# Optimization experiments

Hardware: AMD Instinct MI355X
Metric: run time of the kernel (lower is better)

The kernel has to match this reference:

```python
import jax, jax.numpy as jnp
import numpy as np

TOP_K = 2  # matches init top_k


def setup_inputs() -> dict:
    key = jax.random.key(0)
    k = jax.random.split(key, 5)
    B, S, D, E, H = 8, 2048, 768, 8, 3072  # batch, seq, n_embed, num_experts, 4*n_embed
    init = lambda kk, shape: (jax.random.normal(kk, shape, jnp.float32) * 0.02)
    return {
        "x": jax.random.normal(k[0], (B, S, D), jnp.float32),
        "Wg": init(k[1], (D, E)),            # router weight
        "bg": jnp.zeros((E,), jnp.float32),   # router bias
        "W1": init(k[2], (E, D, H)),          # stacked expert fc1
        "b1": jnp.zeros((E, H), jnp.float32),
        "W2": init(k[3], (E, H, D)),          # stacked expert fc2
        "b2": jnp.zeros((E, D), jnp.float32),
    }


def _moe(x, Wg, bg, W1, b1, W2, b2):
    B, S, D = x.shape
    E = Wg.shape[1]
    # --- TopkRouter: top-k logits, softmax over selected experts, scatter to full gate tensor ---
    logits = x @ Wg + bg                                  # [B,S,E]
    top_vals, top_idx = jax.lax.top_k(logits, TOP_K)      # [B,S,K]
    gates_k = jax.nn.softmax(top_vals, axis=-1)           # softmax over the k selected experts only
    one_hot = jax.nn.one_hot(top_idx, E, dtype=x.dtype)   # [B,S,K,E] (E is small)
    gates = jnp.sum(one_hot * gates_k[..., None], axis=-2)  # [B,S,E], zeros off top-k

    # --- dispatch/compute/combine: scan over experts (fixed, small), gate-weighted accumulate ---
    flat_x = x.reshape(-1, D)          # [T,D]
    flat_g = gates.reshape(-1, E).T    # [E,T]

    def body(acc, p):
        W1e, b1e, W2e, b2e, ge = p
        h = jax.nn.relu(flat_x @ W1e + b1e)               # [T,H]
        acc = acc + (h @ W2e + b2e) * ge[:, None]         # gate==0 -> zero contribution (incl. bias)
        return acc, None

    out, _ = jax.lax.scan(body, jnp.zeros_like(flat_x), (W1, b1, W2, b2, flat_g))
    return out.reshape(B, S, D)


def reference(x, Wg, bg, W1, b1, W2, b2):
    return _moe(x, Wg, bg, W1, b1, W2, b2)
```

## Files before the change

### kernel.cpp

```cpp
#include <hip/hip_runtime.h>
#include <stdint.h>

typedef unsigned short u16;
typedef __attribute__((ext_vector_type(8))) short v8s;
typedef __attribute__((ext_vector_type(4))) float v4f;

#define T_TOK 16384
#define DIM   768
#define NE    8
#define HH    3072
#define CH    1536
#define NCH   2
#define MCAP  34816

#define O_W1T 0u
#define O_W2T 37748736u
#define O_XBF 75497472u
#define O_STK 100663296u
#define O_SGT 100802560u
#define O_TE  100941824u
#define O_TG  101072896u
#define O_TS  101203968u
#define O_MET 101335040u
#define O_HBF 101335296u
#define O_OBF 208290048u
#define WS_TIER_A 261767424ull

__device__ __forceinline__ u16 f2bf(float f){
  uint32_t u = __float_as_uint(f);
  uint32_t r = (u + 0x7fffu + ((u >> 16) & 1u)) >> 16;
  return (u16)r;
}
__device__ __forceinline__ float bf2f(u16 v){
  return __uint_as_float(((uint32_t)v) << 16);
}
__device__ __forceinline__ void gll16(const u16* g, u16* l){
  __builtin_amdgcn_global_load_lds((const __attribute__((address_space(1))) uint32_t*)g,
                                   (__attribute__((address_space(3))) uint32_t*)l, 16, 0, 0);
}

#define BAR() do { asm volatile("" ::: "memory"); __builtin_amdgcn_s_barrier(); asm volatile("" ::: "memory"); } while(0)
#define WAIT_LGKM0() asm volatile("s_waitcnt lgkmcnt(0)" ::: "memory")
#define WAIT_VM4() asm volatile("s_waitcnt vmcnt(4)" ::: "memory")
#define WAIT_VM0() asm volatile("s_waitcnt vmcnt(0)" ::: "memory")

__global__ void k_transposeW1(const float* __restrict__ W1, u16* __restrict__ W1t){
  __shared__ float tile[32][33];
  int e = blockIdx.z;
  int h0 = blockIdx.x * 32, d0 = blockIdx.y * 32;
  const float* src = W1 + (size_t)e * DIM * HH;
  u16* dst = W1t + (size_t)e * HH * DIM;
  int tx = threadIdx.x, ty = threadIdx.y;
  #pragma unroll
  for (int j = 0; j < 4; j++)
    tile[ty + 8*j][tx] = src[(size_t)(d0 + ty + 8*j) * HH + h0 + tx];
  __syncthreads();
  #pragma unroll
  for (int j = 0; j < 4; j++)
    dst[(size_t)(h0 + ty + 8*j) * DIM + d0 + tx] = f2bf(tile[tx][ty + 8*j]);
}

__global__ void k_transposeW2(const float* __restrict__ W2, u16* __restrict__ W2t){
  __shared__ float tile[32][33];
  int e = blockIdx.z;
  int d0 = blockIdx.x * 32, h0 = blockIdx.y * 32;
  const float* src = W2 + (size_t)e * HH * DIM;
  u16* dst = W2t + (size_t)e * DIM * HH;
  int tx = threadIdx.x, ty = threadIdx.y;
  #pragma unroll
  for (int j = 0; j < 4; j++)
    tile[ty + 8*j][tx] = src[(size_t)(h0 + ty + 8*j) * DIM + d0 + tx];
  __syncthreads();
  #pragma unroll
  for (int j = 0; j < 4; j++)
    dst[(size_t)(d0 + ty + 8*j) * HH + h0 + tx] = f2bf(tile[tx][ty + 8*j]);
}

__global__ __launch_bounds__(256) void k_router(
    const float* __restrict__ x, const float* __restrict__ Wg, const float* __restrict__ bg,
    int* __restrict__ tE, float* __restrict__ tG, u16* __restrict__ Xbf){
  int t = blockIdx.x * 4 + (threadIdx.x >> 6);
  int l = threadIdx.x & 63;
  const float* xr = x + (size_t)t * DIM;
  u16* xb = Xbf + (size_t)t * DIM;
  float acc[NE];
  #pragma unroll
  for (int e = 0; e < NE; e++) acc[e] = 0.f;
  #pragma unroll
  for (int j = 0; j < DIM / 64; j++){
    int c = l + 64 * j;
    float xv = xr[c];
    xb[c] = f2bf(xv);
    const float4* wr4 = (const float4*)(Wg + (size_t)c * NE);
    float4 w0 = wr4[0], w1 = wr4[1];
    acc[0] += xv * w0.x; acc[1] += xv * w0.y; acc[2] += xv * w0.z; acc[3] += xv * w0.w;
    acc[4] += xv * w1.x; acc[5] += xv * w1.y; acc[6] += xv * w1.z; acc[7] += xv * w1.w;
  }
  #pragma unroll
  for (int off = 32; off; off >>= 1)
    #pragma unroll
    for (int e = 0; e < NE; e++) acc[e] += __shfl_xor(acc[e], off, 64);

  if (l == 0){
    float lgt[NE];
    #pragma unroll
    for (int e = 0; e < NE; e++) lgt[e] = acc[e] + bg[e];
    int i0 = 0; float v0 = lgt[0];
    #pragma unroll
    for (int e = 1; e < NE; e++) if (lgt[e] > v0){ v0 = lgt[e]; i0 = e; }
    int i1 = -1; float v1 = -1e30f;
    #pragma unroll
    for (int e = 0; e < NE; e++) if (e != i0 && lgt[e] > v1){ v1 = lgt[e]; i1 = e; }
    float ed = expf(v1 - v0);
    float g1 = ed / (1.f + ed);
    float g0 = 1.f / (1.f + ed);
    tE[2*t] = i0; tE[2*t+1] = i1;
    tG[2*t] = g0; tG[2*t+1] = g1;
  }
}

__global__ __launch_bounds__(256) void k_count(const int* __restrict__ tE, int* __restrict__ counts){
  int i = blockIdx.x * blockDim.x + threadIdx.x;
  int c[NE];
  #pragma unroll
  for (int e = 0; e < NE; e++) c[e] = 0;
  for (int j = i; j < 2 * T_TOK; j += 32 * 256){
    int v = tE[j];
    #pragma unroll
    for (int e = 0; e < NE; e++) c[e] += (v == e);
  }
  #pragma unroll
  for (int off = 32; off; off >>= 1)
    #pragma unroll
    for (int e = 0; e < NE; e++) c[e] += __shfl_xor(c[e], off, 64);
  if ((threadIdx.x & 63) == 0){
    #pragma unroll
    for (int e = 0; e < NE; e++) atomicAdd(&counts[e], c[e]);
  }
}

__global__ void k_scan(const int* __restrict__ counts, int* __restrict__ offs){
  if (threadIdx.x == 0){
    int o = 0;
    for (int e = 0; e < NE; e++){ offs[e] = o; o += (counts[e] + 255) & ~255; }
    offs[NE] = o;
  }
}

__global__ __launch_bounds__(256) void k_scatter(
    const int* __restrict__ tE, const float* __restrict__ tG,
    const int* __restrict__ offs, int* __restrict__ fill,
    int* __restrict__ slot_token, float* __restrict__ slot_gate, int* __restrict__ tSlot){
  int t = blockIdx.x * 256 + threadIdx.x;
  int lane = threadIdx.x & 63, w = threadIdx.x >> 6;
  int e0 = tE[2*t], e1 = tE[2*t+1];
  float g0 = tG[2*t], g1 = tG[2*t+1];

  __shared__ int wcnt[4][NE];
  __shared__ int woff[4][NE];
  __shared__ int bbase[NE];

  uint64_t below = (1ull << lane) - 1ull;
  int rank0 = 0, rank1 = 0;
  #pragma unroll
  for (int e = 0; e < NE; e++){
    uint64_t m0 = __ballot(e0 == e);
    uint64_t m1 = __ballot(e1 == e);
    int c0 = __popcll(m0);
    if (e0 == e) rank0 = __popcll(m0 & below);
    if (e1 == e) rank1 = c0 + __popcll(m1 & below);
    if (lane == 0) wcnt[w][e] = c0 + __popcll(m1);
  }
  __syncthreads();
  if (threadIdx.x < NE){
    int e = threadIdx.x;
    int s = 0;
    #pragma unroll
    for (int ww = 0; ww < 4; ww++){ woff[ww][e] = s; s += wcnt[ww][e]; }
    bbase[e] = atomicAdd(&fill[e], s);
  }
  __syncthreads();
  int p0 = offs[e0] + bbase[e0] + woff[w][e0] + rank0;
  slot_token[p0] = t; slot_gate[p0] = g0; tSlot[2*t] = p0;
  int p1 = offs[e1] + bbase[e1] + woff[w][e1] + rank1;
  slot_token[p1] = t; slot_gate[p1] = g1; tSlot[2*t+1] = p1;
}

__global__ void k_outinit(const int* __restrict__ tE, const float* __restrict__ tG,
                          const float* __restrict__ b2, float* __restrict__ out){
  int t = blockIdx.x;
  int e0 = tE[2*t], e1 = tE[2*t+1];
  float g0 = tG[2*t], g1 = tG[2*t+1];
  const float* r0 = b2 + (size_t)e0 * DIM;
  const float* r1 = b2 + (size_t)e1 * DIM;
  float* o = out + (size_t)t * DIM;
  #pragma unroll
  for (int j = 0; j < DIM / 256; j++){
    int c = threadIdx.x + 256 * j;
    o[c] = g0 * r0[c] + g1 * r1[c];
  }
}


#define ABASE(b,h) (((b)*2+(h))*8192)
#define BBASE(b,h) (32768 + ((b)*2+(h))*8192)
#define SWZE(ro,ks) (((((ro)*128) + (ks)*64 + lg*16) ^ (((lm)&7)<<4)) >> 1)

#define STAGE2(p0, p1, base, kk) do { \
  gll16((p0) + (kk), &lds[(base) + (w*2)*512]); \
  gll16((p1) + (kk), &lds[(base) + (w*2+1)*512]); } while(0)

#define MFMA_Q(MOFF, NOFF, BF) \
  __builtin_amdgcn_s_setprio(1); \
  _Pragma("unroll") \
  for (int mi = 0; mi < 4; mi++) \
    _Pragma("unroll") \
    for (int ni = 0; ni < 2; ni++) \
      _Pragma("unroll") \
      for (int ks = 0; ks < 2; ks++) \
        acc[(MOFF)+mi][(NOFF)+ni] = __builtin_amdgcn_mfma_f32_16x16x32_bf16(aF[mi][ks], BF[ni][ks], acc[(MOFF)+mi][(NOFF)+ni], 0, 0, 0); \
  __builtin_amdgcn_s_setprio(0);

__global__ __launch_bounds__(512, 2) void k_gemm1(
    const u16* __restrict__ Xbf, const u16* __restrict__ W1t, const float* __restrict__ b1,
    const int* __restrict__ slot_token, const float* __restrict__ slot_gate,
    const int* __restrict__ offs, u16* __restrict__ Hbuf, int cbase)
{
  const int NT = CH / 256;
  const int NWG = NE * 64 * NT;
  int bid = blockIdx.x;
  int swz = (bid & 7) * (NWG / 8) + (bid >> 3);
  int e = swz / (64 * NT);
  int rem = swz % (64 * NT);
  int mt = rem / NT, ntile = rem % NT;

  int mbase = offs[e];
  int pc = offs[e+1] - mbase;
  if (mt * 256 >= pc) return;
  int grb = mbase + mt * 256;
  int nb = ntile * 256;
  int habs = cbase + nb;

  __shared__ __align__(16) u16 lds[65536];

  int tid = threadIdx.x, w = tid >> 6, lane = tid & 63;
  int wm = w >> 2, wn = w & 3, lm = lane & 15, lg = lane >> 4;
  int cbe = (((lane & 7) ^ (lane >> 3)) << 3);

  int rA00 = (w*2+0)*8 + (lane>>3), rA01 = (w*2+1)*8 + (lane>>3);
  const u16 *sA00 = Xbf + (size_t)slot_token[grb + rA00]       * DIM + cbe;
  const u16 *sA01 = Xbf + (size_t)slot_token[grb + rA01]       * DIM + cbe;
  const u16 *sA10 = Xbf + (size_t)slot_token[grb + 128 + rA00] * DIM + cbe;
  const u16 *sA11 = Xbf + (size_t)slot_token[grb + 128 + rA01] * DIM + cbe;
  const u16 *sB00 = W1t + ((size_t)e*HH + habs + rA00)       * DIM + cbe;
  const u16 *sB01 = W1t + ((size_t)e*HH + habs + rA01)       * DIM + cbe;
  const u16 *sB10 = W1t + ((size_t)e*HH + habs + 128 + rA00) * DIM + cbe;
  const u16 *sB11 = W1t + ((size_t)e*HH + habs + 128 + rA01) * DIM + cbe;

  v4f acc[8][4];
  #pragma unroll
  for (int mi = 0; mi < 8; mi++)
    #pragma unroll
    for (int ni = 0; ni < 4; ni++) acc[mi][ni] = 0.f;

  const int NTK = DIM / 64;
  STAGE2(sA00, sA01, ABASE(0,0), 0);  STAGE2(sA10, sA11, ABASE(0,1), 0);
  STAGE2(sB00, sB01, BBASE(0,0), 0);  STAGE2(sB10, sB11, BBASE(0,1), 0);
  STAGE2(sA00, sA01, ABASE(1,0), 64); STAGE2(sA10, sA11, ABASE(1,1), 64);
  WAIT_VM4(); BAR();

  v8s aF[4][2], bF0[2][2], bF1[2][2];
  for (int k = 0; k < NTK; ++k){
    int cur = k & 1, nx = cur ^ 1;
    int ab = ABASE(cur, wm);
    int bb = BBASE(cur, wn >> 1);
    #pragma unroll
    for (int mi = 0; mi < 4; mi++)
      #pragma unroll
      for (int ks = 0; ks < 2; ks++)
        aF[mi][ks] = *(const v8s*)&lds[ab + SWZE(mi*16 + lm, ks)];
    #pragma unroll
    for (int ni = 0; ni < 2; ni++)
      #pragma unroll
      for (int ks = 0; ks < 2; ks++)
        bF0[ni][ks] = *(const v8s*)&lds[bb + SWZE((wn&1)*64 + ni*16 + lm, ks)];
    if (k + 1 < NTK) STAGE2(sB00, sB01, BBASE(nx,0), (k+1)*64);
    MFMA_Q(0, 0, bF0);
    BAR();
    #pragma unroll
    for (int ni = 0; ni < 2; ni++)
      #pragma unroll
      for (int ks = 0; ks < 2; ks++)
        bF1[ni][ks] = *(const v8s*)&lds[bb + SWZE((wn&1)*64 + (2+ni)*16 + lm, ks)];
    if (k + 1 < NTK) STAGE2(sB10, sB11, BBASE(nx,1), (k+1)*64);
    MFMA_Q(0, 2, bF1);
    BAR();
    #pragma unroll
    for (int mi = 0; mi < 4; mi++)
      #pragma unroll
      for (int ks = 0; ks < 2; ks++)
        aF[mi][ks] = *(const v8s*)&lds[ab + SWZE((4+mi)*16 + lm, ks)];
    MFMA_Q(4, 0, bF0);
    WAIT_LGKM0(); BAR();
    if (k + 2 < NTK){
      STAGE2(sA00, sA01, ABASE(cur,0), (k+2)*64);
      STAGE2(sA10, sA11, ABASE(cur,1), (k+2)*64);
    }
    MFMA_Q(4, 2, bF1);
    if (k + 2 < NTK) { WAIT_VM4(); } else { WAIT_VM0(); }
    BAR();
  }

  float b1v[4];
  #pragma unroll
  for (int ni = 0; ni < 4; ni++) b1v[ni] = b1[(size_t)e * HH + habs + wn*64 + ni*16 + lm];
  #pragma unroll
  for (int mi = 0; mi < 8; mi++){
    int rbase = grb + wm*128 + mi*16 + lg*4;
    float g[4];
    #pragma unroll
    for (int i = 0; i < 4; i++) g[i] = slot_gate[rbase + i];
    #pragma unroll
    for (int ni = 0; ni < 4; ni++){
      int col = nb + wn*64 + ni*16 + lm;
      #pragma unroll
      for (int i = 0; i < 4; i++){
        float v = acc[mi][ni][i] + b1v[ni];
        v = fmaxf(v, 0.f) * g[i];
        Hbuf[(size_t)(rbase + i) * CH + col] = f2bf(v);
      }
    }
  }
}

__global__ __launch_bounds__(512, 2) void k_gemm2(
    const u16* __restrict__ Hbuf, const u16* __restrict__ W2t,
    const int* __restrict__ slot_token, const int* __restrict__ offs,
    float* __restrict__ out, u16* __restrict__ Obuf, int cbase, int mode)
{
  const int NT = DIM / 256;
  const int NWG = NE * 64 * NT;
  int bid = blockIdx.x;
  int swz = (bid & 7) * (NWG / 8) + (bid >> 3);
  int e = swz / (64 * NT);
  int rem = swz % (64 * NT);
  int mt = rem / NT, ntile = rem % NT;

  int mbase = offs[e];
  int pc = offs[e+1] - mbase;
  if (mt * 256 >= pc) return;
  int grb = mbase + mt * 256;
  int nb = ntile * 256;

  __shared__ __align__(16) u16 lds[65536];

  int tid = threadIdx.x, w = tid >> 6, lane = tid & 63;
  int wm = w >> 2, wn = w & 3, lm = lane & 15, lg = lane >> 4;
  int cbe = (((lane & 7) ^ (lane >> 3)) << 3);

  int rA00 = (w*2+0)*8 + (lane>>3), rA01 = (w*2+1)*8 + (lane>>3);
  const u16 *sA00 = Hbuf + (size_t)(grb + rA00)       * CH + cbe;
  const u16 *sA01 = Hbuf + (size_t)(grb + rA01)       * CH + cbe;
  const u16 *sA10 = Hbuf + (size_t)(grb + 128 + rA00) * CH + cbe;
  const u16 *sA11 = Hbuf + (size_t)(grb + 128 + rA01) * CH + cbe;
  const u16 *sB00 = W2t + ((size_t)e*DIM + nb + rA00)       * HH + cbase + cbe;
  const u16 *sB01 = W2t + ((size_t)e*DIM + nb + rA01)       * HH + cbase + cbe;
  const u16 *sB10 = W2t + ((size_t)e*DIM + nb + 128 + rA00) * HH + cbase + cbe;
  const u16 *sB11 = W2t + ((size_t)e*DIM + nb + 128 + rA01) * HH + cbase + cbe;

  v4f acc[8][4];
  #pragma unroll
  for (int mi = 0; mi < 8; mi++)
    #pragma unroll
    for (int ni = 0; ni < 4; ni++) acc[mi][ni] = 0.f;

  const int NTK = CH / 64;
  STAGE2(sA00, sA01, ABASE(0,0), 0);  STAGE2(sA10, sA11, ABASE(0,1), 0);
  STAGE2(sB00, sB01, BBASE(0,0), 0);  STAGE2(sB10, sB11, BBASE(0,1), 0);
  STAGE2(sA00, sA01, ABASE(1,0), 64); STAGE2(sA10, sA11, ABASE(1,1), 64);
  WAIT_VM4(); BAR();

  v8s aF[4][2], bF0[2][2], bF1[2][2];
  for (int k = 0; k < NTK; ++k){
    int cur = k & 1, nx = cur ^ 1;
    int ab = ABASE(cur, wm);
    int bb = BBASE(cur, wn >> 1);
    #pragma unroll
    for (int mi = 0; mi < 4; mi++)
      #pragma unroll
      for (int ks = 0; ks < 2; ks++)
        aF[mi][ks] = *(const v8s*)&lds[ab + SWZE(mi*16 + lm, ks)];
    #pragma unroll
    for (int ni = 0; ni < 2; ni++)
      #pragma unroll
      for (int ks = 0; ks < 2; ks++)
        bF0[ni][ks] = *(const v8s*)&lds[bb + SWZE((wn&1)*64 + ni*16 + lm, ks)];
    if (k + 1 < NTK) STAGE2(sB00, sB01, BBASE(nx,0), (k+1)*64);
    MFMA_Q(0, 0, bF0);
    BAR();
    #pragma unroll
    for (int ni = 0; ni < 2; ni++)
      #pragma unroll
      for (int ks = 0; ks < 2; ks++)
        bF1[ni][ks] = *(const v8s*)&lds[bb + SWZE((wn&1)*64 + (2+ni)*16 + lm, ks)];
    if (k + 1 < NTK) STAGE2(sB10, sB11, BBASE(nx,1), (k+1)*64);
    MFMA_Q(0, 2, bF1);
    BAR();
    #pragma unroll
    for (int mi = 0; mi < 4; mi++)
      #pragma unroll
      for (int ks = 0; ks < 2; ks++)
        aF[mi][ks] = *(const v8s*)&lds[ab + SWZE((4+mi)*16 + lm, ks)];
    MFMA_Q(4, 0, bF0);
    WAIT_LGKM0(); BAR();
    if (k + 2 < NTK){
      STAGE2(sA00, sA01, ABASE(cur,0), (k+2)*64);
      STAGE2(sA10, sA11, ABASE(cur,1), (k+2)*64);
    }
    MFMA_Q(4, 2, bF1);
    if (k + 2 < NTK) { WAIT_VM4(); } else { WAIT_VM0(); }
    BAR();
  }

  if (mode == 0){
    #pragma unroll
    for (int mi = 0; mi < 8; mi++){
      int rbase = grb + wm*128 + mi*16 + lg*4;
      int tok[4];
      #pragma unroll
      for (int i = 0; i < 4; i++) tok[i] = slot_token[rbase + i];
      #pragma unroll
      for (int ni = 0; ni < 4; ni++){
        int col = nb + wn*64 + ni*16 + lm;
        #pragma unroll
        for (int i = 0; i < 4; i++)
          unsafeAtomicAdd(&out[(size_t)tok[i] * DIM + col], acc[mi][ni][i]);
      }
    }
  } else if (mode == 1){
    #pragma unroll
    for (int mi = 0; mi < 8; mi++){
      int rbase = grb + wm*128 + mi*16 + lg*4;
      #pragma unroll
      for (int ni = 0; ni < 4; ni++){
        int col = nb + wn*64 + ni*16 + lm;
        #pragma unroll
        for (int i = 0; i < 4; i++)
          Obuf[(size_t)(rbase + i) * DIM + col] = f2bf(acc[mi][ni][i]);
      }
    }
  } else {
    #pragma unroll
    for (int mi = 0; mi < 8; mi++){
      int rbase = grb + wm*128 + mi*16 + lg*4;
      #pragma unroll
      for (int ni = 0; ni < 4; ni++){
        int col = nb + wn*64 + ni*16 + lm;
        #pragma unroll
        for (int i = 0; i < 4; i++){
          size_t p = (size_t)(rbase + i) * DIM + col;
          Obuf[p] = f2bf(bf2f(Obuf[p]) + acc[mi][ni][i]);
        }
      }
    }
  }
}

__global__ __launch_bounds__(192) void k_combine(
    const u16* __restrict__ Obuf, const int* __restrict__ tSlot,
    const int* __restrict__ tE, const float* __restrict__ tG,
    const float* __restrict__ b2, float* __restrict__ out)
{
  int t = blockIdx.x;
  int l = threadIdx.x;
  int s0 = tSlot[2*t], s1 = tSlot[2*t+1];
  int e0 = tE[2*t], e1 = tE[2*t+1];
  float g0 = tG[2*t], g1 = tG[2*t+1];
  int c = l * 4;
  ushort4 a = *(const ushort4*)(Obuf + (size_t)s0 * DIM + c);
  ushort4 b = *(const ushort4*)(Obuf + (size_t)s1 * DIM + c);
  float4 bA = *(const float4*)(b2 + (size_t)e0 * DIM + c);
  float4 bB = *(const float4*)(b2 + (size_t)e1 * DIM + c);
  float4 r;
  r.x = bf2f(a.x) + bf2f(b.x) + g0 * bA.x + g1 * bB.x;
  r.y = bf2f(a.y) + bf2f(b.y) + g0 * bA.y + g1 * bB.y;
  r.z = bf2f(a.z) + bf2f(b.z) + g0 * bA.z + g1 * bB.z;
  r.w = bf2f(a.w) + bf2f(b.w) + g0 * bA.w + g1 * bB.w;
  *(float4*)(out + (size_t)t * DIM + c) = r;
}

extern "C" void kernel_launch(void* const* d_in, const int* in_sizes, int n_in,
                              void* d_out, int out_size, void* d_ws, size_t ws_size,
                              hipStream_t stream)
{
  const float* x  = (const float*)d_in[0];
  const float* Wg = (const float*)d_in[1];
  const float* bg = (const float*)d_in[2];
  const float* W1 = (const float*)d_in[3];
  const float* b1 = (const float*)d_in[4];
  const float* W2 = (const float*)d_in[5];
  const float* b2 = (const float*)d_in[6];
  float* out = (float*)d_out;
  char* ws = (char*)d_ws;

  u16*   W1t        = (u16*)(ws + O_W1T);
  u16*   W2t        = (u16*)(ws + O_W2T);
  u16*   Xbf        = (u16*)(ws + O_XBF);
  u16*   Hbuf       = (u16*)(ws + O_HBF);
  u16*   Obuf       = (u16*)(ws + O_OBF);
  int*   slot_token = (int*)(ws + O_STK);
  float* slot_gate  = (float*)(ws + O_SGT);
  int*   tE         = (int*)(ws + O_TE);
  float* tG         = (float*)(ws + O_TG);
  int*   tSlot      = (int*)(ws + O_TS);
  int*   meta       = (int*)(ws + O_MET);
  int*   counts = meta;
  int*   fill   = meta + 8;
  int*   offs   = meta + 16;

  const bool tierA = (ws_size >= WS_TIER_A);

  hipMemsetAsync(ws + O_STK, 0, O_TE - O_STK, stream);
  hipMemsetAsync(ws + O_MET, 0, 128, stream);

  k_transposeW1<<<dim3(HH/32, DIM/32, NE), dim3(32, 8), 0, stream>>>(W1, W1t);
  k_transposeW2<<<dim3(DIM/32, HH/32, NE), dim3(32, 8), 0, stream>>>(W2, W2t);

  k_router<<<T_TOK/4, 256, 0, stream>>>(x, Wg, bg, tE, tG, Xbf);
  k_count<<<32, 256, 0, stream>>>(tE, counts);
  k_scan<<<1, 1, 0, stream>>>(counts, offs);
  k_scatter<<<T_TOK/256, 256, 0, stream>>>(tE, tG, offs, fill, slot_token, slot_gate, tSlot);
  if (!tierA)
    k_outinit<<<T_TOK, 256, 0, stream>>>(tE, tG, b2, out);

  for (int c = 0; c < NCH; c++){
    k_gemm1<<<NE * 64 * (CH/256), 512, 0, stream>>>(Xbf, W1t, b1, slot_token, slot_gate, offs, Hbuf, c * CH);
    int mode = tierA ? (c == 0 ? 1 : 2) : 0;
    k_gemm2<<<NE * 64 * (DIM/256), 512, 0, stream>>>(Hbuf, W2t, slot_token, offs, out, Obuf, c * CH, mode);
  }
  if (tierA)
    k_combine<<<T_TOK, 192, 0, stream>>>(Obuf, tSlot, tE, tG, b2, out);
}
```

Baseline: 487.8 us.

## Use compact flat M-tile grid and single-pass full-H GEMMs when workspace allows

Replaces the per-expert 64-tile grid (most blocks exiting early) with a flat grid over the padded slot array, locating each tile's expert from the offsets. When the workspace is large enough, GEMM1 and GEMM2 each run once over the full hidden dimension instead of in two chunks, with a matching Obuf layout. This cuts empty-block launch overhead and halves kernel launches and tail effects, but needs a larger H buffer and assumes each expert's slot range is padded to 256-row alignment so a tile never spans two experts.

New measurement: 492.6 us. No clear change (+1.0%).

```diff
diff --git a/kernel.cpp b/kernel.cpp
--- a/kernel.cpp
+++ b/kernel.cpp
@@ -9,9 +9,8 @@
 #define DIM   768
 #define NE    8
 #define HH    3072
-#define CH    1536
-#define NCH   2
 #define MCAP  34816
+#define GM    (MCAP/256)
 
 #define O_W1T 0u
 #define O_W2T 37748736u
@@ -23,8 +22,11 @@
 #define O_TS  101203968u
 #define O_MET 101335040u
 #define O_HBF 101335296u
-#define O_OBF 208290048u
-#define WS_TIER_A 261767424ull
+#define HBF_A2 213909504u
+#define HBF_A  106954752u
+#define OBF_SZ 53477376u
+#define WS_TIER_A2 (O_HBF + HBF_A2 + OBF_SZ)
+#define WS_TIER_A  (O_HBF + HBF_A  + OBF_SZ)
 
 __device__ __forceinline__ u16 f2bf(float f){
   uint32_t u = __float_as_uint(f);
@@ -221,23 +223,29 @@
         acc[(MOFF)+mi][(NOFF)+ni] = __builtin_amdgcn_mfma_f32_16x16x32_bf16(aF[mi][ks], BF[ni][ks], acc[(MOFF)+mi][(NOFF)+ni], 0, 0, 0); \
   __builtin_amdgcn_s_setprio(0);
 
+__device__ __forceinline__ int find_expert(const int* offs, int grb, int& total){
+  int offr[NE+1];
+  #pragma unroll
+  for (int i = 0; i <= NE; i++) offr[i] = offs[i];
+  total = offr[NE];
+  int e = 0;
+  #pragma unroll
+  for (int i = 1; i < NE; i++) e += (grb >= offr[i]);
+  return e;
+}
+
 __global__ __launch_bounds__(512, 2) void k_gemm1(
     const u16* __restrict__ Xbf, const u16* __restrict__ W1t, const float* __restrict__ b1,
     const int* __restrict__ slot_token, const float* __restrict__ slot_gate,
-    const int* __restrict__ offs, u16* __restrict__ Hbuf, int cbase)
+    const int* __restrict__ offs, u16* __restrict__ Hbuf, int hs, int cbase, int ntc)
 {
-  const int NT = CH / 256;
-  const int NWG = NE * 64 * NT;
   int bid = blockIdx.x;
-  int swz = (bid & 7) * (NWG / 8) + (bid >> 3);
-  int e = swz / (64 * NT);
-  int rem = swz % (64 * NT);
-  int mt = rem / NT, ntile = rem % NT;
-
-  int mbase = offs[e];
-  int pc = offs[e+1] - mbase;
-  if (mt * 256 >= pc) return;
-  int grb = mbase + mt * 256;
+  int swz = (bid & 7) * ((int)gridDim.x >> 3) + (bid >> 3);
+  int mt = swz / ntc, ntile = swz % ntc;
+  int grb = mt * 256;
+  int total;
+  int e = find_expert(offs, grb, total);
+  if (grb >= total) return;
   int nb = ntile * 256;
   int habs = cbase + nb;
 
@@ -327,7 +335,7 @@
       for (int i = 0; i < 4; i++){
         float v = acc[mi][ni][i] + b1v[ni];
         v = fmaxf(v, 0.f) * g[i];
-        Hbuf[(size_t)(rbase + i) * CH + col] = f2bf(v);
+        Hbuf[(size_t)(rbase + i) * hs + col] = f2bf(v);
       }
     }
   }
@@ -336,20 +344,16 @@
 __global__ __launch_bounds__(512, 2) void k_gemm2(
     const u16* __restrict__ Hbuf, const u16* __restrict__ W2t,
     const int* __restrict__ slot_token, const int* __restrict__ offs,
-    float* __restrict__ out, u16* __restrict__ Obuf, int cbase, int mode)
+    float* __restrict__ out, u16* __restrict__ Obuf, int hs, int cbase, int klen, int mode)
 {
   const int NT = DIM / 256;
-  const int NWG = NE * 64 * NT;
   int bid = blockIdx.x;
-  int swz = (bid & 7) * (NWG / 8) + (bid >> 3);
-  int e = swz / (64 * NT);
-  int rem = swz % (64 * NT);
-  int mt = rem / NT, ntile = rem % NT;
-
-  int mbase = offs[e];
-  int pc = offs[e+1] - mbase;
-  if (mt * 256 >= pc) return;
-  int grb = mbase + mt * 256;
+  int swz = (bid & 7) * ((int)gridDim.x >> 3) + (bid >> 3);
+  int mt = swz / NT, ntile = swz % NT;
+  int grb = mt * 256;
+  int total;
+  int e = find_expert(offs, grb, total);
+  if (grb >= total) return;
   int nb = ntile * 256;
 
   __shared__ __align__(16) u16 lds[65536];
@@ -359,10 +363,10 @@
   int cbe = (((lane & 7) ^ (lane >> 3)) << 3);
 
   int rA00 = (w*2+0)*8 + (lane>>3), rA01 = (w*2+1)*8 + (lane>>3);
-  const u16 *sA00 = Hbuf + (size_t)(grb + rA00)       * CH + cbe;
-  const u16 *sA01 = Hbuf + (size_t)(grb + rA01)       * CH + cbe;
-  const u16 *sA10 = Hbuf + (size_t)(grb + 128 + rA00) * CH + cbe;
-  const u16 *sA11 = Hbuf + (size_t)(grb + 128 + rA01) * CH + cbe;
+  const u16 *sA00 = Hbuf + (size_t)(grb + rA00)       * hs + cbe;
+  const u16 *sA01 = Hbuf + (size_t)(grb + rA01)       * hs + cbe;
+  const u16 *sA10 = Hbuf + (size_t)(grb + 128 + rA00) * hs + cbe;
+  const u16 *sA11 = Hbuf + (size_t)(grb + 128 + rA01) * hs + cbe;
   const u16 *sB00 = W2t + ((size_t)e*DIM + nb + rA00)       * HH + cbase + cbe;
   const u16 *sB01 = W2t + ((size_t)e*DIM + nb + rA01)       * HH + cbase + cbe;
   const u16 *sB10 = W2t + ((size_t)e*DIM + nb + 128 + rA00) * HH + cbase + cbe;
@@ -374,14 +378,14 @@
     #pragma unroll
     for (int ni = 0; ni < 4; ni++) acc[mi][ni] = 0.f;
 
-  const int NTK = CH / 64;
+  const int ntk = klen / 64;
   STAGE2(sA00, sA01, ABASE(0,0), 0);  STAGE2(sA10, sA11, ABASE(0,1), 0);
   STAGE2(sB00, sB01, BBASE(0,0), 0);  STAGE2(sB10, sB11, BBASE(0,1), 0);
   STAGE2(sA00, sA01, ABASE(1,0), 64); STAGE2(sA10, sA11, ABASE(1,1), 64);
   WAIT_VM4(); BAR();
 
   v8s aF[4][2], bF0[2][2], bF1[2][2];
-  for (int k = 0; k < NTK; ++k){
+  for (int k = 0; k < ntk; ++k){
     int cur = k & 1, nx = cur ^ 1;
     int ab = ABASE(cur, wm);
     int bb = BBASE(cur, wn >> 1);
@@ -395,7 +399,7 @@
       #pragma unroll
       for (int ks = 0; ks < 2; ks++)
         bF0[ni][ks] = *(const v8s*)&lds[bb + SWZE((wn&1)*64 + ni*16 + lm, ks)];
-    if (k + 1 < NTK) STAGE2(sB00, sB01, BBASE(nx,0), (k+1)*64);
+    if (k + 1 < ntk) STAGE2(sB00, sB01, BBASE(nx,0), (k+1)*64);
     MFMA_Q(0, 0, bF0);
     BAR();
     #pragma unroll
@@ -403,7 +407,7 @@
       #pragma unroll
       for (int ks = 0; ks < 2; ks++)
         bF1[ni][ks] = *(const v8s*)&lds[bb + SWZE((wn&1)*64 + (2+ni)*16 + lm, ks)];
-    if (k + 1 < NTK) STAGE2(sB10, sB11, BBASE(nx,1), (k+1)*64);
+    if (k + 1 < ntk) STAGE2(sB10, sB11, BBASE(nx,1), (k+1)*64);
     MFMA_Q(0, 2, bF1);
     BAR();
     #pragma unroll
@@ -413,12 +417,12 @@
         aF[mi][ks] = *(const v8s*)&lds[ab + SWZE((4+mi)*16 + lm, ks)];
     MFMA_Q(4, 0, bF0);
     WAIT_LGKM0(); BAR();
-    if (k + 2 < NTK){
+    if (k + 2 < ntk){
       STAGE2(sA00, sA01, ABASE(cur,0), (k+2)*64);
       STAGE2(sA10, sA11, ABASE(cur,1), (k+2)*64);
     }
     MFMA_Q(4, 2, bF1);
-    if (k + 2 < NTK) { WAIT_VM4(); } else { WAIT_VM0(); }
+    if (k + 2 < ntk) { WAIT_VM4(); } else { WAIT_VM0(); }
     BAR();
   }
 
@@ -507,7 +511,6 @@
   u16*   W2t        = (u16*)(ws + O_W2T);
   u16*   Xbf        = (u16*)(ws + O_XBF);
   u16*   Hbuf       = (u16*)(ws + O_HBF);
-  u16*   Obuf       = (u16*)(ws + O_OBF);
   int*   slot_token = (int*)(ws + O_STK);
   float* slot_gate  = (float*)(ws + O_SGT);
   int*   tE         = (int*)(ws + O_TE);
@@ -518,7 +521,9 @@
   int*   fill   = meta + 8;
   int*   offs   = meta + 16;
 
-  const bool tierA = (ws_size >= WS_TIER_A);
+  const int tier = (ws_size >= WS_TIER_A2) ? 2 : (ws_size >= WS_TIER_A) ? 1 : 0;
+  const unsigned hbf_sz = (tier == 2) ? HBF_A2 : HBF_A;
+  u16* Obuf = (u16*)(ws + O_HBF + hbf_sz);
 
   hipMemsetAsync(ws + O_STK, 0, O_TE - O_STK, stream);
   hipMemsetAsync(ws + O_MET, 0, 128, stream);
@@ -530,14 +535,21 @@
   k_count<<<32, 256, 0, stream>>>(tE, counts);
   k_scan<<<1, 1, 0, stream>>>(counts, offs);
   k_scatter<<<T_TOK/256, 256, 0, stream>>>(tE, tG, offs, fill, slot_token, slot_gate, tSlot);
-  if (!tierA)
+  if (tier == 0)
     k_outinit<<<T_TOK, 256, 0, stream>>>(tE, tG, b2, out);
 
-  for (int c = 0; c < NCH; c++){
-    k_gemm1<<<NE * 64 * (CH/256), 512, 0, stream>>>(Xbf, W1t, b1, slot_token, slot_gate, offs, Hbuf, c * CH);
-    int mode = tierA ? (c == 0 ? 1 : 2) : 0;
-    k_gemm2<<<NE * 64 * (DIM/256), 512, 0, stream>>>(Hbuf, W2t, slot_token, offs, out, Obuf, c * CH, mode);
-  }
-  if (tierA)
+  if (tier == 2){
+    k_gemm1<<<GM * (HH/256), 512, 0, stream>>>(Xbf, W1t, b1, slot_token, slot_gate, offs, Hbuf, HH, 0, HH/256);
+    k_gemm2<<<GM * (DIM/256), 512, 0, stream>>>(Hbuf, W2t, slot_token, offs, out, Obuf, HH, 0, HH, 1);
     k_combine<<<T_TOK, 192, 0, stream>>>(Obuf, tSlot, tE, tG, b2, out);
-}
+  } else {
+    const int CH = 1536;
+    for (int c = 0; c < 2; c++){
+      k_gemm1<<<GM * (CH/256), 512, 0, stream>>>(Xbf, W1t, b1, slot_token, slot_gate, offs, Hbuf, CH, c*CH, CH/256);
+      int mode = (tier == 1) ? (c == 0 ? 1 : 2) : 0;
+      k_gemm2<<<GM * (DIM/256), 512, 0, stream>>>(Hbuf, W2t, slot_token, offs, out, Obuf, CH, c*CH, CH, mode);
+    }
+    if (tier == 1)
+      k_combine<<<T_TOK, 192, 0, stream>>>(Obuf, tSlot, tE, tG, b2, out);
+  }
+}
```
